# Kernel optimization log

Hardware: AMD Instinct MI355X
Metric: run time of the kernel (lower is better)

The kernel has to match this reference:

```python
import jax, jax.numpy as jnp
import numpy as np
from jax import lax

EPS = 1e-6

def _ln(x):
    # LayerNorm32 over channel dim, computed in fp32
    x32 = x.astype(jnp.float32)
    mu = jnp.mean(x32, axis=-1, keepdims=True)
    var = jnp.mean(jnp.square(x32 - mu), axis=-1, keepdims=True)
    return ((x32 - mu) * lax.rsqrt(var + EPS)).astype(x.dtype)

def _downsample2(f, mask):
    # mean over active voxels in each 2x2x2 cell; f must already be zero at inactive voxels
    B, D, H, W, C = f.shape
    fs = f.reshape(B, D // 2, 2, H // 2, 2, W // 2, 2, C).sum(axis=(2, 4, 6))
    cnt = mask.reshape(B, D // 2, 2, H // 2, 2, W // 2, 2).astype(f.dtype).sum(axis=(2, 4, 6))
    out = fs / jnp.maximum(cnt, 1.0)[..., None]
    return out, cnt > 0

def _subm_conv3(x, w, b, mask_f):
    # submanifold sparse conv == dense SAME conv on zero-filled grid, masked to active set
    y = lax.conv_general_dilated(x, w, window_strides=(1, 1, 1), padding='SAME',
                                 dimension_numbers=('NDHWC', 'DHWIO', 'NDHWC'))
    return (y + b) * mask_f


def setup_inputs() -> dict:
    key = jax.random.key(0)
    ks = jax.random.split(key, 6)
    B, D, C, CO = 4, 64, 64, 128
    feats = jax.random.normal(ks[0], (B, D, D, D, C), jnp.float32)
    mask = jax.random.uniform(ks[1], (B, D, D, D)) < 0.3
    gamma1 = jnp.ones((C,), jnp.float32)
    beta1 = jnp.zeros((C,), jnp.float32)
    w1 = jax.random.normal(ks[2], (3, 3, 3, C, CO), jnp.float32) / np.sqrt(27.0 * C)
    b1 = jnp.zeros((CO,), jnp.float32)
    # conv2 is zero-initialized in the original (zero_module); we use small random
    # weights so the reference is numerically non-degenerate
    w2 = jax.random.normal(ks[3], (3, 3, 3, CO, CO), jnp.float32) / np.sqrt(27.0 * CO)
    b2 = jnp.zeros((CO,), jnp.float32)
    w_skip = jax.random.normal(ks[4], (C, CO), jnp.float32) / np.sqrt(C)
    b_skip = jnp.zeros((CO,), jnp.float32)
    return dict(feats=feats, mask=mask, gamma1=gamma1, beta1=beta1,
                w1=w1, b1=b1, w2=w2, b2=b2, w_skip=w_skip, b_skip=b_skip)


def reference(feats, mask, gamma1, beta1, w1, b1, w2, b2, w_skip, b_skip):
    m = mask[..., None].astype(feats.dtype)          # [B,D,H,W,1]
    h = (_ln(feats) * gamma1 + beta1)                # norm1 (affine)
    h = jax.nn.silu(h) * m                           # silu, restrict to active set
    xm = feats * m
    h, mask2 = _downsample2(h, mask)                 # SparseDownsample(2) on h
    x_ds, _ = _downsample2(xm, mask)                 # SparseDownsample(2) on x
    m2 = mask2[..., None].astype(feats.dtype)
    h = _subm_conv3(h, w1, b1, m2)                   # conv1
    h = jax.nn.silu(_ln(h)) * m2                     # norm2 (no affine) + silu
    h = _subm_conv3(h, w2, b2, m2)                   # conv2
    skip = (x_ds @ w_skip + b_skip) * m2             # SparseLinear skip
    return h + skip
```

## Files before the change

kernel.cpp:

```cpp
#include <hip/hip_runtime.h>
#include <hip/hip_bf16.h>

#define EPS 1e-6f
typedef unsigned short b16;
typedef __attribute__((ext_vector_type(8))) short v8s;
typedef __attribute__((ext_vector_type(4))) float v4f;

__device__ __forceinline__ b16 f2b(float f) {
    __hip_bfloat16 h = __float2bfloat16(f);
    return *reinterpret_cast<b16*>(&h);
}
__device__ __forceinline__ float siluf(float x){ return x / (1.f + __expf(-x)); }

template<int IC>
__global__ void __launch_bounds__(256) k_wt(const float* __restrict__ w, b16* __restrict__ o, int tot) {
    int i = blockIdx.x*256 + threadIdx.x;
    if (i >= tot) return;
    int ic = i % IC; int oc = (i / IC) & 127; int tap = i / (IC*128);
    o[i] = f2b(w[(tap*IC + ic)*128 + oc]);
}

template<int IC>
__global__ void __launch_bounds__(256) k_wtb(const float* __restrict__ w, b16* __restrict__ o, int tot) {
    int i = blockIdx.x*256 + threadIdx.x;
    if (i >= tot) return;
    constexpr int ICB = IC/32;
    int icl = i & 31;
    int oc  = (i >> 5) & 127;
    int r   = i >> 12;
    int tap = r / ICB, icb = r % ICB;
    o[i] = f2b(w[(tap*IC + icb*32 + icl)*128 + oc]);
}

__global__ void __launch_bounds__(256) k_ln_down(
    const float* __restrict__ feats, const int* __restrict__ mask,
    const float* __restrict__ gamma, const float* __restrict__ beta,
    b16* __restrict__ h_ds_pad, b16* __restrict__ x_ds, float* __restrict__ cnt_out)
{
    int wave = (blockIdx.x * 256 + threadIdx.x) >> 6;
    int lane = threadIdx.x & 63;
    int x = wave & 31, y = (wave >> 5) & 31, z = (wave >> 10) & 31, b = wave >> 15;
    float g = gamma[lane], be = beta[lane];
    float hacc = 0.f, xacc = 0.f, cnt = 0.f;
    #pragma unroll
    for (int i = 0; i < 8; ++i) {
        int zz = 2*z + (i>>2), yy = 2*y + ((i>>1)&1), xx = 2*x + (i&1);
        int vox = ((b*64 + zz)*64 + yy)*64 + xx;
        int m = mask[vox];
        float val = feats[vox*64 + lane];
        float s1 = val, s2 = val*val;
        #pragma unroll
        for (int off = 32; off > 0; off >>= 1) {
            s1 += __shfl_xor(s1, off, 64);
            s2 += __shfl_xor(s2, off, 64);
        }
        float mu = s1 * (1.f/64.f);
        float var = fmaxf(s2 * (1.f/64.f) - mu*mu, 0.f);
        float h = (val - mu) * rsqrtf(var + EPS) * g + be;
        h = siluf(h);
        if (m != 0) { hacc += h; xacc += val; cnt += 1.f; }
    }
    float inv = 1.f / fmaxf(cnt, 1.f);
    long vp = ((long)(b*34 + z+1)*34 + (y+1))*34 + (x+1);
    h_ds_pad[vp*64 + lane] = f2b(hacc * inv);
    x_ds[(long)wave*64 + lane] = f2b(xacc * inv);
    if (lane == 0) cnt_out[wave] = cnt;
}

template<int IC, bool IS_CONV1>
__global__ void __launch_bounds__(256) k_conv_mfma(
    const b16* __restrict__ inp,
    const b16* __restrict__ wt,
    const float* __restrict__ bias,
    const float* __restrict__ cnt,
    const b16* __restrict__ x_ds,
    const b16* __restrict__ wst,
    const float* __restrict__ b_skip,
    b16* __restrict__ h2out,
    float* __restrict__ out)
{
    constexpr int ICB = IC/32;
    constexpr int NK = 27*ICB;
    __shared__ b16 lA[4096];
    __shared__ b16 lB[4096];

    int bid = blockIdx.x;
    int y0 = (bid & 7) << 2;
    int z  = (bid >> 3) & 31;
    int b  = bid >> 8;
    int t  = threadIdx.x;
    int lane = t & 63;
    int w = t >> 6;
    int col = lane & 15;
    int quad = lane >> 4;

    int av = t >> 1, ac = (t & 1) << 1;
    int ayr = av >> 5, ax = av & 31;
    const b16* gA = inp + ((long)((b*34 + z)*34 + (y0 + ayr))*34 + ax)*IC + ac*8;
    int lA0 = av*32 + ((ac     + (ax>>1)) & 3)*8;
    int lA1 = av*32 + ((ac + 1 + (ax>>1)) & 3)*8;
    int ocs = t >> 1, bc = (t & 1) << 1;
    const b16* gB = wt + ocs*32 + bc*8;
    int lB0 = ocs*32 + ((bc     + ((ocs&15)>>1)) & 3)*8;
    int lB1 = ocs*32 + ((bc + 1 + ((ocs&15)>>1)) & 3)*8;

    int so   = ((quad + (col>>1)) & 3) * 8;
    int aoff = w*1024 + col*32 + so;
    int boff = col*32 + so;

    v4f acc[2][8];
    #pragma unroll
    for (int tl=0;tl<2;++tl)
        #pragma unroll
        for (int n=0;n<8;++n) acc[tl][n] = (v4f){0.f,0.f,0.f,0.f};

    v8s ra0 = *(const v8s*)(gA);
    v8s ra1 = *(const v8s*)(gA + 8);
    v8s rb0 = *(const v8s*)(gB);
    v8s rb1 = *(const v8s*)(gB + 8);

    for (int k = 0; k < NK; ++k) {
        *(v8s*)(lA + lA0) = ra0;
        *(v8s*)(lA + lA1) = ra1;
        *(v8s*)(lB + lB0) = rb0;
        *(v8s*)(lB + lB1) = rb1;
        __syncthreads();
        if (k + 1 < NK) {
            int kn = k + 1;
            int tap = kn / ICB, icb = kn & (ICB-1);
            int kz = tap / 9, rr = tap - kz*9;
            int ky = rr / 3, kx = rr - ky*3;
            long off = ((long)(kz*34 + ky)*34 + kx)*IC + icb*32;
            ra0 = *(const v8s*)(gA + off);
            ra1 = *(const v8s*)(gA + off + 8);
            const b16* gBk = gB + (long)kn*4096;
            rb0 = *(const v8s*)(gBk);
            rb1 = *(const v8s*)(gBk + 8);
        }
        v8s a0 = *(const v8s*)(lA + aoff);
        v8s a1 = *(const v8s*)(lA + aoff + 512);
        #pragma unroll
        for (int n = 0; n < 8; ++n) {
            v8s bb = *(const v8s*)(lB + n*512 + boff);
            acc[0][n] = __builtin_amdgcn_mfma_f32_16x16x32_bf16(a0, bb, acc[0][n], 0,0,0);
            acc[1][n] = __builtin_amdgcn_mfma_f32_16x16x32_bf16(a1, bb, acc[1][n], 0,0,0);
        }
        __syncthreads();
    }

    int yrow = y0 + w;
    long cellrow = ((long)(b*32+z)*32 + yrow)*32;

    if (!IS_CONV1) {
        const b16* X0 = x_ds + (cellrow + col)*64 + quad*8;
        const b16* X1 = X0 + 16*64;
        const b16* WS = wst + col*64 + quad*8;
        #pragma unroll
        for (int s = 0; s < 2; ++s) {
            v8s a0 = *(const v8s*)(X0 + s*32);
            v8s a1 = *(const v8s*)(X1 + s*32);
            #pragma unroll
            for (int n=0;n<8;++n) {
                v8s bb = *(const v8s*)(WS + n*16*64 + s*32);
                acc[0][n] = __builtin_amdgcn_mfma_f32_16x16x32_bf16(a0, bb, acc[0][n], 0,0,0);
                acc[1][n] = __builtin_amdgcn_mfma_f32_16x16x32_bf16(a1, bb, acc[1][n], 0,0,0);
            }
        }
    }

    float bv[8];
    #pragma unroll
    for (int n=0;n<8;++n)
        bv[n] = bias[n*16+col] + (IS_CONV1 ? 0.f : b_skip[n*16+col]);

    long prow = ((long)(b*34 + z+1)*34 + (yrow+1))*34 + 1;

    #pragma unroll
    for (int tl=0; tl<2; ++tl) {
        if (IS_CONV1) {
            float s1[4], s2[4];
            #pragma unroll
            for (int r=0;r<4;++r){
                float a=0.f, q=0.f;
                #pragma unroll
                for (int n=0;n<8;++n){ float v = acc[tl][n][r] + bv[n]; a+=v; q+=v*v; }
                s1[r]=a; s2[r]=q;
            }
            #pragma unroll
            for (int off=1; off<16; off<<=1){
                #pragma unroll
                for (int r=0;r<4;++r){ s1[r]+=__shfl_xor(s1[r],off); s2[r]+=__shfl_xor(s2[r],off); }
            }
            #pragma unroll
            for (int r=0;r<4;++r){
                int row = quad*4 + r;
                int x = tl*16 + row;
                float c = cnt[cellrow + x];
                float mu = s1[r]*(1.f/128.f);
                float var = fmaxf(s2[r]*(1.f/128.f) - mu*mu, 0.f);
                float rs = rsqrtf(var + EPS);
                bool act = c > 0.f;
                #pragma unroll
                for (int n=0;n<8;++n){
                    float v = acc[tl][n][r] + bv[n];
                    float hv = act ? siluf((v-mu)*rs) : 0.f;
                    h2out[(prow + x)*128 + n*16 + col] = f2b(hv);
                }
            }
        } else {
            #pragma unroll
            for (int r=0;r<4;++r){
                int row = quad*4 + r;
                int x = tl*16 + row;
                float c = cnt[cellrow + x];
                bool act = c > 0.f;
                #pragma unroll
                for (int n=0;n<8;++n){
                    float v = acc[tl][n][r] + bv[n];
                    out[(cellrow + x)*128 + n*16 + col] = act ? v : 0.f;
                }
            }
        }
    }
}

extern "C" void kernel_launch(void* const* d_in, const int* in_sizes, int n_in,
                              void* d_out, int out_size, void* d_ws, size_t ws_size,
                              hipStream_t stream) {
    const float* feats  = (const float*)d_in[0];
    const int*   mask   = (const int*)  d_in[1];
    const float* gamma1 = (const float*)d_in[2];
    const float* beta1  = (const float*)d_in[3];
    const float* w1     = (const float*)d_in[4];
    const float* b1     = (const float*)d_in[5];
    const float* w2     = (const float*)d_in[6];
    const float* b2     = (const float*)d_in[7];
    const float* w_skip = (const float*)d_in[8];
    const float* b_skip = (const float*)d_in[9];
    float* out = (float*)d_out;

    char* ws = (char*)d_ws;
    b16*   h_ds_pad = (b16*)(ws);
    b16*   h2_pad   = (b16*)(ws + 20123648);
    b16*   x_ds     = (b16*)(ws + 60370944);
    float* cnt      = (float*)(ws + 77148160);
    b16*   w1t      = (b16*)(ws + 77672448);
    b16*   w2t      = (b16*)(ws + 78114816);
    b16*   wst      = (b16*)(ws + 78999552);

    hipMemsetAsync(h_ds_pad, 0, 20123648, stream);
    hipMemsetAsync(h2_pad,   0, 40247296, stream);

    const int n_w1 = 27*64*128;
    const int n_w2 = 27*128*128;
    const int n_ws = 64*128;
    k_wtb<64> <<<(n_w1 + 255)/256, 256, 0, stream>>>(w1, w1t, n_w1);
    k_wtb<128><<<(n_w2 + 255)/256, 256, 0, stream>>>(w2, w2t, n_w2);
    k_wt<64>  <<<(n_ws + 255)/256, 256, 0, stream>>>(w_skip, wst, n_ws);

    k_ln_down<<<32768, 256, 0, stream>>>(feats, mask, gamma1, beta1, h_ds_pad, x_ds, cnt);

    k_conv_mfma<64,true><<<1024, 256, 0, stream>>>(h_ds_pad, w1t, b1, cnt,
                                                   nullptr, nullptr, nullptr,
                                                   h2_pad, nullptr);
    k_conv_mfma<128,false><<<1024, 256, 0, stream>>>(h2_pad, w2t, b2, cnt,
                                                     x_ds, wst, b_skip,
                                                     nullptr, out);
}
```

Baseline: 705.9 us.

## Double-buffer conv LDS tiles with direct global-to-LDS loads

Replaces the register-staged global loads and LDS stores in the implicit-GEMM conv loop with global_load_lds direct transfers into a double-buffered LDS tile. Swizzle offsets are now folded into the global source addresses, and the tap offset is advanced incrementally instead of being recomputed with divisions. One barrier per iteration is removed and s_setprio is raised around the MFMA block. The aim is to overlap the next tile's fetch with the current MFMAs and cut VGPR and ALU overhead, at the cost of twice the LDS per block, which could lower occupancy. Correctness depends on the loads completing before the barrier.

```diff
diff --git a/kernel.cpp b/kernel.cpp
--- a/kernel.cpp
+++ b/kernel.cpp
@@ -6,11 +6,18 @@
 typedef __attribute__((ext_vector_type(8))) short v8s;
 typedef __attribute__((ext_vector_type(4))) float v4f;
 
+typedef const __attribute__((address_space(1))) void* gptr_t;
+typedef __attribute__((address_space(3))) void* lptr_t;
+
 __device__ __forceinline__ b16 f2b(float f) {
     __hip_bfloat16 h = __float2bfloat16(f);
     return *reinterpret_cast<b16*>(&h);
 }
 __device__ __forceinline__ float siluf(float x){ return x / (1.f + __expf(-x)); }
+
+__device__ __forceinline__ void gll16(const b16* g, b16* l) {
+    __builtin_amdgcn_global_load_lds((gptr_t)g, (lptr_t)l, 16, 0, 0);
+}
 
 template<int IC>
 __global__ void __launch_bounds__(256) k_wt(const float* __restrict__ w, b16* __restrict__ o, int tot) {
@@ -81,8 +88,8 @@
 {
     constexpr int ICB = IC/32;
     constexpr int NK = 27*ICB;
-    __shared__ b16 lA[4096];
-    __shared__ b16 lB[4096];
+    __shared__ b16 lA[2][4096];
+    __shared__ b16 lB[2][4096];
 
     int bid = blockIdx.x;
     int y0 = (bid & 7) << 2;
@@ -94,15 +101,21 @@
     int col = lane & 15;
     int quad = lane >> 4;
 
-    int av = t >> 1, ac = (t & 1) << 1;
-    int ayr = av >> 5, ax = av & 31;
-    const b16* gA = inp + ((long)((b*34 + z)*34 + (y0 + ayr))*34 + ax)*IC + ac*8;
-    int lA0 = av*32 + ((ac     + (ax>>1)) & 3)*8;
-    int lA1 = av*32 + ((ac + 1 + (ax>>1)) & 3)*8;
-    int ocs = t >> 1, bc = (t & 1) << 1;
-    const b16* gB = wt + ocs*32 + bc*8;
-    int lB0 = ocs*32 + ((bc     + ((ocs&15)>>1)) & 3)*8;
-    int lB1 = ocs*32 + ((bc + 1 + ((ocs&15)>>1)) & 3)*8;
+    const b16* gAsrc[2];
+    const b16* gBsrc[2];
+    {
+        int vsub = lane >> 2;
+        int s    = lane & 3;
+        #pragma unroll
+        for (int j = 0; j < 2; ++j) {
+            int x  = j*16 + vsub;
+            int cA = (s - (x >> 1)) & 3;
+            gAsrc[j] = inp + ((long)((b*34 + z)*34 + (y0 + w))*34 + x)*IC + cA*8;
+            int oc = w*32 + j*16 + vsub;
+            int cB = (s - (vsub >> 1)) & 3;
+            gBsrc[j] = wt + oc*32 + cB*8;
+        }
+    }
 
     int so   = ((quad + (col>>1)) & 3) * 8;
     int aoff = w*1024 + col*32 + so;
@@ -114,38 +127,53 @@
         #pragma unroll
         for (int n=0;n<8;++n) acc[tl][n] = (v4f){0.f,0.f,0.f,0.f};
 
-    v8s ra0 = *(const v8s*)(gA);
-    v8s ra1 = *(const v8s*)(gA + 8);
-    v8s rb0 = *(const v8s*)(gB);
-    v8s rb1 = *(const v8s*)(gB + 8);
-
+    long offAn = 0;
+    int icbn = 0, kxn = 0, kyn = 0;
+    auto advance = [&]() {
+        ++icbn; offAn += 32;
+        if (icbn == ICB) {
+            icbn = 0;
+            ++kxn;
+            if (kxn == 3) {
+                kxn = 0; ++kyn;
+                if (kyn == 3) { kyn = 0; offAn += (long)(34*34 - 2*34 - 3)*IC; }
+                else          {           offAn += (long)(34 - 3)*IC; }
+            }
+        }
+    };
+
+    auto stage = [&](long offA, long offB, int buf) {
+        #pragma unroll
+        for (int j = 0; j < 2; ++j) {
+            gll16(gAsrc[j] + offA, &lA[buf][w*1024 + j*512]);
+            gll16(gBsrc[j] + offB, &lB[buf][w*1024 + j*512]);
+        }
+    };
+
+    stage(0, 0, 0);
+    advance();
+    long offBn = 4096;
+    __syncthreads();
+
+    int cur = 0;
     for (int k = 0; k < NK; ++k) {
-        *(v8s*)(lA + lA0) = ra0;
-        *(v8s*)(lA + lA1) = ra1;
-        *(v8s*)(lB + lB0) = rb0;
-        *(v8s*)(lB + lB1) = rb1;
-        __syncthreads();
         if (k + 1 < NK) {
-            int kn = k + 1;
-            int tap = kn / ICB, icb = kn & (ICB-1);
-            int kz = tap / 9, rr = tap - kz*9;
-            int ky = rr / 3, kx = rr - ky*3;
-            long off = ((long)(kz*34 + ky)*34 + kx)*IC + icb*32;
-            ra0 = *(const v8s*)(gA + off);
-            ra1 = *(const v8s*)(gA + off + 8);
-            const b16* gBk = gB + (long)kn*4096;
-            rb0 = *(const v8s*)(gBk);
-            rb1 = *(const v8s*)(gBk + 8);
-        }
-        v8s a0 = *(const v8s*)(lA + aoff);
-        v8s a1 = *(const v8s*)(lA + aoff + 512);
+            stage(offAn, offBn, cur ^ 1);
+            advance();
+            offBn += 4096;
+        }
+        v8s a0 = *(const v8s*)(&lA[cur][aoff]);
+        v8s a1 = *(const v8s*)(&lA[cur][aoff + 512]);
+        __builtin_amdgcn_s_setprio(1);
         #pragma unroll
         for (int n = 0; n < 8; ++n) {
-            v8s bb = *(const v8s*)(lB + n*512 + boff);
+            v8s bb = *(const v8s*)(&lB[cur][n*512 + boff]);
             acc[0][n] = __builtin_amdgcn_mfma_f32_16x16x32_bf16(a0, bb, acc[0][n], 0,0,0);
             acc[1][n] = __builtin_amdgcn_mfma_f32_16x16x32_bf16(a1, bb, acc[1][n], 0,0,0);
         }
+        __builtin_amdgcn_s_setprio(0);
         __syncthreads();
+        cur ^= 1;
     }
 
     int yrow = y0 + w;
```

Measured after the change: 734.0 us. +4.0%, slower.
